# Kernel optimization log

Measured on AMD Instinct MI355X. Metric: run time of the kernel, lower is better.

The kernel has to match this reference:

```python
import jax, jax.numpy as jnp
import numpy as np

B, T, IN_DIM, HID, OUT_DIM = 256, 512, 128, 512, 128


def _lstm_cell(x, h, c, W_ih, W_hh, b_ih, b_hh):
    # torch LSTMCell gate order: i, f, g, o
    gates = x @ W_ih.T + h @ W_hh.T + (b_ih + b_hh)  # [B, 4H]
    i, f, g, o = jnp.split(gates, 4, axis=-1)
    i = jax.nn.sigmoid(i)
    f = jax.nn.sigmoid(f)
    g = jnp.tanh(g)
    o = jax.nn.sigmoid(o)
    c_new = f * c + i * g
    h_new = o * jnp.tanh(c_new)
    return h_new, c_new


def setup_inputs() -> dict:
    key = jax.random.key(0)
    ks = jax.random.split(key, 12)
    s1 = 1.0 / np.sqrt(HID)
    inp = {
        "input_tensor": jax.random.normal(ks[0], (B, T, IN_DIM), dtype=jnp.float32),
        "future": 0,
        "W_ih1": jax.random.uniform(ks[1], (4 * HID, IN_DIM), jnp.float32, -s1, s1),
        "W_hh1": jax.random.uniform(ks[2], (4 * HID, HID), jnp.float32, -s1, s1),
        "b_ih1": jax.random.uniform(ks[3], (4 * HID,), jnp.float32, -s1, s1),
        "b_hh1": jax.random.uniform(ks[4], (4 * HID,), jnp.float32, -s1, s1),
        "W_ih2": jax.random.uniform(ks[5], (4 * HID, HID), jnp.float32, -s1, s1),
        "W_hh2": jax.random.uniform(ks[6], (4 * HID, HID), jnp.float32, -s1, s1),
        "b_ih2": jax.random.uniform(ks[7], (4 * HID,), jnp.float32, -s1, s1),
        "b_hh2": jax.random.uniform(ks[8], (4 * HID,), jnp.float32, -s1, s1),
        "W_lin": jax.random.uniform(ks[9], (OUT_DIM, HID), jnp.float32, -s1, s1),
        "b_lin": jax.random.uniform(ks[10], (OUT_DIM,), jnp.float32, -s1, s1),
    }
    return inp


def reference(input_tensor, future, W_ih1, W_hh1, b_ih1, b_hh1,
              W_ih2, W_hh2, b_ih2, b_hh2, W_lin, b_lin):
    Bsz = input_tensor.shape[0]
    H = W_hh1.shape[1]
    zeros = jnp.zeros((Bsz, H), dtype=input_tensor.dtype)
    init = (zeros, zeros, zeros, zeros)  # h1, c1, h2, c2

    def step(carry, x_t):
        h1, c1, h2, c2 = carry
        h1, c1 = _lstm_cell(x_t, h1, c1, W_ih1, W_hh1, b_ih1, b_hh1)
        h2, c2 = _lstm_cell(h1, h2, c2, W_ih2, W_hh2, b_ih2, b_hh2)
        out = h2 @ W_lin.T + b_lin  # [B, out_dim]
        return (h1, c1, h2, c2), out

    xs = jnp.swapaxes(input_tensor, 0, 1)  # [T, B, in_dim]
    carry, outs = jax.lax.scan(step, init, xs)  # outs: [T, B, out]
    outputs = jnp.swapaxes(outs, 0, 1)  # [B, T, out]

    if future > 0:
        def fstep(carry, _):
            h1, c1, h2, c2, prev = carry
            h1, c1 = _lstm_cell(prev, h1, c1, W_ih1, W_hh1, b_ih1, b_hh1)
            h2, c2 = _lstm_cell(h1, h2, c2, W_ih2, W_hh2, b_ih2, b_hh2)
            out = h2 @ W_lin.T + b_lin
            return (h1, c1, h2, c2, out), out
        fcarry = (*carry, outputs[:, -1, :])
        _, fouts = jax.lax.scan(fstep, fcarry, None, length=future)
        outputs = jnp.concatenate([outputs, jnp.swapaxes(fouts, 0, 1)], axis=1)

    # torch .squeeze(2): no-op unless out_dim == 1
    if outputs.shape[2] == 1:
        outputs = outputs[:, :, 0]
    return outputs
```

## Files before the change

kernel.cpp:

```cpp
#include <hip/hip_runtime.h>


#define Bsz 256
#define Tsz 512
#define INsz 128
#define Hsz 512
#define OUTsz 128

typedef _Float16 half8 __attribute__((ext_vector_type(8)));
typedef float f32x16 __attribute__((ext_vector_type(16)));
typedef float f32x4 __attribute__((ext_vector_type(4)));
typedef unsigned int u32x4 __attribute__((ext_vector_type(4)));
typedef unsigned long long u64;

#define ROWP 520
#define HBU 65536u

#define H1S_B 0
#define H2S_B 32768
#define XS_B  65536
#define GEXA_B 73728
#define GEXB_B 110592
#define LDS1_SIZE 147456
#define LDS2_SIZE 133120

__device__ __forceinline__ float sigm(float v)   { return 1.0f / (1.0f + __expf(-v)); }
__device__ __forceinline__ float tanh_f(float v) { return 2.0f / (1.0f + __expf(-2.0f * v)) - 1.0f; }

__device__ __forceinline__ half8 load_w8(const float* src) {
  f32x4 a = *(const f32x4*)src;
  f32x4 b = *(const f32x4*)(src + 4);
  half8 v;
  v[0] = (_Float16)a[0]; v[1] = (_Float16)a[1]; v[2] = (_Float16)a[2]; v[3] = (_Float16)a[3];
  v[4] = (_Float16)b[0]; v[5] = (_Float16)b[1]; v[6] = (_Float16)b[2]; v[7] = (_Float16)b[3];
  return v;
}

__device__ __forceinline__ void dump_acc(float* gex, const f32x16& acc, int blk, int nloc, int ktop) {
  #pragma unroll
  for (int r4 = 0; r4 < 4; ++r4) {
    f32x4 v;
    v[0] = acc[r4*4+0]; v[1] = acc[r4*4+1]; v[2] = acc[r4*4+2]; v[3] = acc[r4*4+3];
    *(f32x4*)(gex + (blk*32 + nloc)*36 + r4*8 + ktop*4) = v;
  }
}

__device__ __forceinline__ void epilogue_gates(const float* gex, int eb, int ed,
                                               float bi, float bf, float bg, float bo,
                                               float& c, float& hout) {
  float gi = bi, gf = bf, gg = bg, go = bo;
  #pragma unroll
  for (int q = 0; q < 4; ++q) {
    gi += gex[(q*32 + ed)*36 + eb];
    gf += gex[(q*32 + ed + 16)*36 + eb];
    gg += gex[((4+q)*32 + ed)*36 + eb];
    go += gex[((4+q)*32 + ed + 16)*36 + eb];
  }
  float ii = sigm(gi), ff = sigm(gf), ta = tanh_f(gg), oo = sigm(go);
  c = ff * c + ii * ta;
  hout = oo * tanh_f(c);
}

__device__ __forceinline__ unsigned h_bits(float h) {
  union { _Float16 f; unsigned short u; } cv;
  cv.f = (_Float16)h;
  return (unsigned)cv.u;
}

__device__ __forceinline__ u64 load_u64_sc0(const u64* p) {
  u64 v;
  asm volatile("global_load_dwordx2 %0, %1, off sc0" : "=v"(v) : "v"(p));
  return v;
}

__global__ void __launch_bounds__(512, 2) lstm_seq(
    const float* __restrict__ x,
    const float* __restrict__ Wih1, const float* __restrict__ Whh1,
    const float* __restrict__ bih1, const float* __restrict__ bhh1,
    const float* __restrict__ Wih2, const float* __restrict__ Whh2,
    const float* __restrict__ bih2, const float* __restrict__ bhh2,
    unsigned int* cnt_base,
    unsigned int* __restrict__ hbuf1, unsigned int* __restrict__ hbuf2,
    unsigned int* __restrict__ h2hist)
{
  extern __shared__ char lds[];
  float* gexA = (float*)(lds + GEXA_B);
  float* gexB = (float*)(lds + GEXB_B);
  int* s_gw = (int*)(lds + GEXA_B);

  const int tid  = threadIdx.x;
  const int lane = tid & 63;
  const int wv   = tid >> 6;
  const int tq   = wv & 1;
  const int kq   = wv >> 1;
  const int blk  = tq * 4 + kq;

  if (tid == 0) {
    unsigned xcd = __builtin_amdgcn_s_getreg(6164) & 7u;
    unsigned slot = __hip_atomic_fetch_add(cnt_base + 512 + xcd, 1u,
                                           __ATOMIC_RELAXED, __HIP_MEMORY_SCOPE_AGENT);
    s_gw[0] = (int)xcd;
    s_gw[1] = (int)(slot & 31u);
  }
  __syncthreads();
  const int g = s_gw[0];
  const int w = s_gw[1];
  __syncthreads();

  unsigned int* cnt = cnt_base + g * 64;

  const int nloc  = lane & 31;
  const int ktop  = lane >> 5;
  const int gtype = tq * 2 + (nloc >> 4);
  const int wdim  = w * 16 + (nloc & 15);
  const int grow  = gtype * 512 + wdim;

  half8 wA[10], wB[16];
  #pragma unroll
  for (int s = 0; s < 8; ++s)
    wA[s] = load_w8(Whh1 + (size_t)grow * Hsz + (kq*8 + s)*16 + ktop*8);
  #pragma unroll
  for (int s = 0; s < 2; ++s)
    wA[8+s] = load_w8(Wih1 + (size_t)grow * INsz + kq*32 + s*16 + ktop*8);
  #pragma unroll
  for (int s = 0; s < 8; ++s)
    wB[s] = load_w8(Wih2 + (size_t)grow * Hsz + (kq*8 + s)*16 + ktop*8);
  #pragma unroll
  for (int s = 0; s < 8; ++s)
    wB[8+s] = load_w8(Whh2 + (size_t)grow * Hsz + (kq*8 + s)*16 + ktop*8);

  const int ed = tid & 15;
  const int eb = tid >> 4;
  const int edim = w * 16 + ed;
  float bi1 = bih1[0*512+edim] + bhh1[0*512+edim];
  float bf1 = bih1[1*512+edim] + bhh1[1*512+edim];
  float bg1 = bih1[2*512+edim] + bhh1[2*512+edim];
  float bo1 = bih1[3*512+edim] + bhh1[3*512+edim];
  float bi2 = bih2[0*512+edim] + bhh2[0*512+edim];
  float bf2 = bih2[1*512+edim] + bhh2[1*512+edim];
  float bg2 = bih2[2*512+edim] + bhh2[2*512+edim];
  float bo2 = bih2[3*512+edim] + bhh2[3*512+edim];
  float c1 = 0.0f, c2 = 0.0f;

  const int stg_m = tid >> 4, stg_ch = tid & 15;
  const int fragC = (kq*8)*32 + ktop*16;
  const int xC    = kq*64 + ktop*16;

  for (int i = 0; i <= Tsz; ++i) {
    const bool doA = (i < Tsz);
    const bool doB = (i > 0);

    const u64* pb1 = (const u64*)hbuf1 + (size_t)((i+1)&1)*32768 + g*4096;
    const u64* pb2 = (const u64*)hbuf2 + (size_t)(i&1)*32768 + g*4096;
    unsigned* wb1 = hbuf1 + (i&1)*HBU;
    unsigned* wb2 = hbuf2 + ((i+1)&1)*HBU;

    u64 q1[8], q2[8];
    #pragma unroll
    for (int j = 0; j < 8; ++j)
      q1[j] = load_u64_sc0(pb1 + j*512 + tid);
    if (doB) {
      #pragma unroll
      for (int j = 0; j < 8; ++j)
        q2[j] = load_u64_sc0(pb2 + j*512 + tid);
    }
    if (doA) {
      const float* src = x + ((size_t)(g*32 + stg_m) * Tsz + i) * INsz + stg_ch*8;
      *(half8*)(lds + XS_B + stg_m*256 + ((stg_ch*16) ^ ((stg_m & 15) << 4))) = load_w8(src);
    }
    asm volatile("s_waitcnt vmcnt(0)" ::: "memory");
    __builtin_amdgcn_sched_barrier(0);
    #pragma unroll
    for (int j = 0; j < 8; ++j) {
      const int L = j*512 + tid, r = L >> 7, b = (L & 127) * 8;
      *(u64*)(lds + H1S_B + r*1024 + (b ^ (r << 4))) = q1[j];
    }
    if (doB) {
      #pragma unroll
      for (int j = 0; j < 8; ++j) {
        const int L = j*512 + tid, r = L >> 7, b = (L & 127) * 8;
        *(u64*)(lds + H2S_B + r*1024 + (b ^ (r << 4))) = q2[j];
      }
    }
    __syncthreads();

    half8 a1[8];
    #pragma unroll
    for (int s = 0; s < 8; ++s)
      a1[s] = *(const half8*)(lds + H1S_B + nloc*1024 + ((fragC + s*32) ^ (nloc << 4)));

    if (doA) {
      f32x16 acc;
      #pragma unroll
      for (int k = 0; k < 16; ++k) acc[k] = 0.0f;
      #pragma unroll
      for (int s = 0; s < 8; ++s)
        acc = __builtin_amdgcn_mfma_f32_32x32x16_f16(a1[s], wA[s], acc, 0, 0, 0);
      #pragma unroll
      for (int s = 0; s < 2; ++s) {
        half8 ax = *(const half8*)(lds + XS_B + nloc*256 + ((xC + s*32) ^ ((nloc & 15) << 4)));
        acc = __builtin_amdgcn_mfma_f32_32x32x16_f16(ax, wA[8+s], acc, 0, 0, 0);
      }
      dump_acc(gexA, acc, blk, nloc, ktop);
    }
    if (doB) {
      f32x16 acc;
      #pragma unroll
      for (int k = 0; k < 16; ++k) acc[k] = 0.0f;
      #pragma unroll
      for (int s = 0; s < 8; ++s)
        acc = __builtin_amdgcn_mfma_f32_32x32x16_f16(a1[s], wB[s], acc, 0, 0, 0);
      #pragma unroll
      for (int s = 0; s < 8; ++s) {
        half8 a2 = *(const half8*)(lds + H2S_B + nloc*1024 + ((fragC + s*32) ^ (nloc << 4)));
        acc = __builtin_amdgcn_mfma_f32_32x32x16_f16(a2, wB[8+s], acc, 0, 0, 0);
      }
      dump_acc(gexB, acc, blk, nloc, ktop);
    }
    __syncthreads();

    if (doA) {
      float h;
      epilogue_gates(gexA, eb, ed, bi1, bf1, bg1, bo1, c1, h);
      unsigned lo = h_bits(h);
      unsigned hi = __shfl_down(lo, 1, 64);
      if (!(tid & 1))
        wb1[((g*32 + eb)*Hsz + w*16 + ed) >> 1] = lo | (hi << 16);
    }
    if (doB) {
      float h;
      epilogue_gates(gexB, eb, ed, bi2, bf2, bg2, bo2, c2, h);
      unsigned lo = h_bits(h);
      unsigned hi = __shfl_down(lo, 1, 64);
      if (!(tid & 1)) {
        unsigned v = lo | (hi << 16);
        wb2[((g*32 + eb)*Hsz + w*16 + ed) >> 1] = v;
        __builtin_nontemporal_store(v,
            h2hist + ((((size_t)(g*32 + eb)*Tsz + (i-1))*Hsz + w*16 + ed) >> 1));
      }
    }
    if (i == Tsz) break;

    __syncthreads();
    if (tid == 0) {
      __hip_atomic_fetch_add(cnt, 1u, __ATOMIC_RELAXED, __HIP_MEMORY_SCOPE_AGENT);
      const unsigned target = (unsigned)(i + 1) * 32u;
      while (__hip_atomic_load(cnt, __ATOMIC_RELAXED, __HIP_MEMORY_SCOPE_AGENT) < target)
        __builtin_amdgcn_s_sleep(1);
    }
    __syncthreads();
  }
}

__global__ void __launch_bounds__(256) out_gemm(
    const _Float16* __restrict__ h2hist, const float* __restrict__ Wlin,
    const float* __restrict__ blin, float* __restrict__ out)
{
  extern __shared__ char lds[];
  _Float16* As = (_Float16*)lds;
  _Float16* Bs = (_Float16*)(lds + 66560);
  const int tid = threadIdx.x;
  const int bt0 = blockIdx.x * 64;
  const int n0  = blockIdx.y * 64;

  {
    const int r = tid >> 2, k0 = (tid & 3) * 128;
    const u32x4* src = (const u32x4*)(h2hist + (size_t)(bt0 + r) * Hsz + k0);
    #pragma unroll
    for (int i = 0; i < 16; ++i)
      *(u32x4*)(As + r*ROWP + k0 + i*8) = src[i];
  }
  {
    const int n = tid >> 2, k0 = (tid & 3) * 128;
    const float* src = Wlin + (size_t)(n0 + n) * Hsz + k0;
    #pragma unroll
    for (int i = 0; i < 16; ++i)
      *(half8*)(Bs + n*ROWP + k0 + i*8) = load_w8(src + i*8);
  }
  __syncthreads();

  const int lane = tid & 63;
  const int wvid = tid >> 6;
  const int mrow = wvid*16 + (lane & 15);
  const int kt   = lane >> 4;
  f32x4 acc[4];
  #pragma unroll
  for (int nt = 0; nt < 4; ++nt) { acc[nt][0]=0; acc[nt][1]=0; acc[nt][2]=0; acc[nt][3]=0; }

  #pragma unroll
  for (int ks = 0; ks < 16; ++ks) {
    half8 a = *(const half8*)(As + mrow*ROWP + ks*32 + kt*8);
    #pragma unroll
    for (int nt = 0; nt < 4; ++nt) {
      half8 b = *(const half8*)(Bs + (nt*16 + (lane & 15))*ROWP + ks*32 + kt*8);
      acc[nt] = __builtin_amdgcn_mfma_f32_16x16x32_f16(a, b, acc[nt], 0, 0, 0);
    }
  }
  #pragma unroll
  for (int nt = 0; nt < 4; ++nt) {
    const int n = n0 + nt*16 + (lane & 15);
    const float bb = blin[n];
    #pragma unroll
    for (int r = 0; r < 4; ++r) {
      const int row = bt0 + wvid*16 + (lane >> 4)*4 + r;
      out[(size_t)row * OUTsz + n] = acc[nt][r] + bb;
    }
  }
}

extern "C" void kernel_launch(void* const* d_in, const int* in_sizes, int n_in,
                              void* d_out, int out_size, void* d_ws, size_t ws_size,
                              hipStream_t stream) {
  const float* x    = (const float*)d_in[0];
  const float* Wih1 = (const float*)d_in[2];
  const float* Whh1 = (const float*)d_in[3];
  const float* bih1 = (const float*)d_in[4];
  const float* bhh1 = (const float*)d_in[5];
  const float* Wih2 = (const float*)d_in[6];
  const float* Whh2 = (const float*)d_in[7];
  const float* bih2 = (const float*)d_in[8];
  const float* bhh2 = (const float*)d_in[9];
  const float* Wlin = (const float*)d_in[10];
  const float* blin = (const float*)d_in[11];
  float* out = (float*)d_out;

  char* ws = (char*)d_ws;
  unsigned int* cnt    = (unsigned int*)ws;
  unsigned int* hbuf1  = (unsigned int*)(ws + 4096);
  unsigned int* hbuf2  = (unsigned int*)(ws + 4096 + 524288);
  unsigned int* h2hist = (unsigned int*)(ws + 2097152);

  hipMemsetAsync(ws, 0, 4096 + 1048576, stream);

  hipFuncSetAttribute((const void*)lstm_seq, hipFuncAttributeMaxDynamicSharedMemorySize, LDS1_SIZE);
  hipFuncSetAttribute((const void*)out_gemm, hipFuncAttributeMaxDynamicSharedMemorySize, LDS2_SIZE);

  void* args[] = { (void*)&x, (void*)&Wih1, (void*)&Whh1, (void*)&bih1, (void*)&bhh1,
                   (void*)&Wih2, (void*)&Whh2, (void*)&bih2, (void*)&bhh2,
                   (void*)&cnt, (void*)&hbuf1, (void*)&hbuf2, (void*)&h2hist };
  hipLaunchCooperativeKernel((const void*)lstm_seq, dim3(256), dim3(512), args,
                             (unsigned int)LDS1_SIZE, stream);

  out_gemm<<<dim3(2048, 2), dim3(256), LDS2_SIZE, stream>>>((const _Float16*)h2hist, Wlin, blin, out);
}
```

Measured before the change: 2.768 ms.

## Replace atomic counter barrier with per-block flags and prefetch next-step input

```diff
diff --git a/kernel.cpp b/kernel.cpp
--- a/kernel.cpp
+++ b/kernel.cpp
@@ -70,6 +70,12 @@
 __device__ __forceinline__ u64 load_u64_sc0(const u64* p) {
   u64 v;
   asm volatile("global_load_dwordx2 %0, %1, off sc0" : "=v"(v) : "v"(p));
+  return v;
+}
+__device__ __forceinline__ unsigned load_u32_sc0_wait(const unsigned* p) {
+  unsigned v;
+  asm volatile("global_load_dword %0, %1, off sc0\n\ts_waitcnt vmcnt(0)"
+               : "=v"(v) : "v"(p) : "memory");
   return v;
 }
 
@@ -97,7 +103,7 @@
 
   if (tid == 0) {
     unsigned xcd = __builtin_amdgcn_s_getreg(6164) & 7u;
-    unsigned slot = __hip_atomic_fetch_add(cnt_base + 512 + xcd, 1u,
+    unsigned slot = __hip_atomic_fetch_add(cnt_base + 1024 + xcd, 1u,
                                            __ATOMIC_RELAXED, __HIP_MEMORY_SCOPE_AGENT);
     s_gw[0] = (int)xcd;
     s_gw[1] = (int)(slot & 31u);
@@ -107,7 +113,8 @@
   const int w = s_gw[1];
   __syncthreads();
 
-  unsigned int* cnt = cnt_base + g * 64;
+  unsigned int* flags_llc = cnt_base + g * 64;
+  unsigned int* flags_l2  = cnt_base + 512 + g * 64;
 
   const int nloc  = lane & 31;
   const int ktop  = lane >> 5;
@@ -143,8 +150,12 @@
   float c1 = 0.0f, c2 = 0.0f;
 
   const int stg_m = tid >> 4, stg_ch = tid & 15;
+  const int xs_off = XS_B + stg_m*256 + ((stg_ch*16) ^ ((stg_m & 15) << 4));
   const int fragC = (kq*8)*32 + ktop*16;
   const int xC    = kq*64 + ktop*16;
+
+  *(half8*)(lds + xs_off) =
+      load_w8(x + ((size_t)(g*32 + stg_m) * Tsz + 0) * INsz + stg_ch*8);
 
   for (int i = 0; i <= Tsz; ++i) {
     const bool doA = (i < Tsz);
@@ -164,10 +175,6 @@
       for (int j = 0; j < 8; ++j)
         q2[j] = load_u64_sc0(pb2 + j*512 + tid);
     }
-    if (doA) {
-      const float* src = x + ((size_t)(g*32 + stg_m) * Tsz + i) * INsz + stg_ch*8;
-      *(half8*)(lds + XS_B + stg_m*256 + ((stg_ch*16) ^ ((stg_m & 15) << 4))) = load_w8(src);
-    }
     asm volatile("s_waitcnt vmcnt(0)" ::: "memory");
     __builtin_amdgcn_sched_barrier(0);
     #pragma unroll
@@ -218,6 +225,14 @@
       dump_acc(gexB, acc, blk, nloc, ktop);
     }
     __syncthreads();
+
+    const bool doX = (i + 1 < Tsz);
+    f32x4 xa, xb;
+    if (doX) {
+      const float* src = x + ((size_t)(g*32 + stg_m) * Tsz + (i+1)) * INsz + stg_ch*8;
+      xa = *(const f32x4*)src;
+      xb = *(const f32x4*)(src + 4);
+    }
 
     if (doA) {
       float h;
@@ -242,11 +257,35 @@
     if (i == Tsz) break;
 
     __syncthreads();
+
+    if (doX) {
+      half8 v;
+      v[0] = (_Float16)xa[0]; v[1] = (_Float16)xa[1]; v[2] = (_Float16)xa[2]; v[3] = (_Float16)xa[3];
+      v[4] = (_Float16)xb[0]; v[5] = (_Float16)xb[1]; v[6] = (_Float16)xb[2]; v[7] = (_Float16)xb[3];
+      *(half8*)(lds + xs_off) = v;
+    }
+
     if (tid == 0) {
-      __hip_atomic_fetch_add(cnt, 1u, __ATOMIC_RELAXED, __HIP_MEMORY_SCOPE_AGENT);
-      const unsigned target = (unsigned)(i + 1) * 32u;
-      while (__hip_atomic_load(cnt, __ATOMIC_RELAXED, __HIP_MEMORY_SCOPE_AGENT) < target)
-        __builtin_amdgcn_s_sleep(1);
+      flags_l2[w] = (unsigned)(i + 1);
+      __hip_atomic_store(flags_llc + w, (unsigned)(i + 1),
+                         __ATOMIC_RELAXED, __HIP_MEMORY_SCOPE_AGENT);
+    }
+    if (wv == 0) {
+      const unsigned target = (unsigned)(i + 1);
+      bool done = false;
+      #pragma unroll 1
+      for (int it = 0; it < 48 && !done; ++it) {
+        unsigned v = (lane < 32) ? load_u32_sc0_wait(flags_l2 + lane) : target;
+        done = __all((int)(v >= target));
+      }
+      #pragma unroll 1
+      while (!done) {
+        unsigned v = (lane < 32)
+            ? __hip_atomic_load(flags_llc + lane, __ATOMIC_RELAXED, __HIP_MEMORY_SCOPE_AGENT)
+            : target;
+        done = __all((int)(v >= target));
+        if (!done) __builtin_amdgcn_s_sleep(1);
+      }
     }
     __syncthreads();
   }
@@ -326,11 +365,11 @@
 
   char* ws = (char*)d_ws;
   unsigned int* cnt    = (unsigned int*)ws;
-  unsigned int* hbuf1  = (unsigned int*)(ws + 4096);
-  unsigned int* hbuf2  = (unsigned int*)(ws + 4096 + 524288);
+  unsigned int* hbuf1  = (unsigned int*)(ws + 8192);
+  unsigned int* hbuf2  = (unsigned int*)(ws + 8192 + 524288);
   unsigned int* h2hist = (unsigned int*)(ws + 2097152);
 
-  hipMemsetAsync(ws, 0, 4096 + 1048576, stream);
+  hipMemsetAsync(ws, 0, 8192 + 1048576, stream);
 
   hipFuncSetAttribute((const void*)lstm_seq, hipFuncAttributeMaxDynamicSharedMemorySize, LDS1_SIZE);
   hipFuncSetAttribute((const void*)out_gemm, hipFuncAttributeMaxDynamicSharedMemorySize, LDS2_SIZE);
```

Measured after the change: 4.707 ms. 70.1% more time.
